# Kernel tuning notes

Hardware: AMD Instinct MI355X
Metric: run time of the kernel (lower is better)

Reference implementation:

```python
import jax, jax.numpy as jnp
import numpy as np

DECAY = 0.1
ALPHA = 0.2
EPS = 1e-8


def setup_inputs() -> dict:
    key = jax.random.key(0)
    k1, k2, k3, k4 = jax.random.split(key, 4)
    B, S, N, V = 8, 1024, 64, 32000
    input_ids = jax.random.randint(k1, (B, S), 0, V)
    emb = jax.random.normal(k2, (V, N), dtype=jnp.float32)
    W = jax.random.normal(k3, (N, N, N), dtype=jnp.float32) * 0.05
    Wd = jax.random.normal(k4, (V, N), dtype=jnp.float32) * 0.02
    bd = jnp.zeros((V,), dtype=jnp.float32)
    return {"input_ids": input_ids, "emb": emb, "W": W, "Wd": Wd, "bd": bd}


def reference(input_ids, emb, W, Wd, bd):
    B, S = input_ids.shape
    N = W.shape[0]
    # Precompute relu(embedding) for all timesteps: [B, S, N]
    word = jax.nn.relu(emb[input_ids])

    def step(hidden, w_t):
        # hidden, w_t: [B, N]
        x = (1.0 - DECAY) * hidden + w_t
        interaction = jnp.einsum('ijk,bi,bj->bk', W, x, x)
        x_act = jax.nn.relu(x + ALPHA * interaction)
        h = x_act / (jnp.sum(x_act, axis=1, keepdims=True) + EPS)
        return h, h

    h0 = jnp.zeros((B, N), dtype=emb.dtype)
    hT, hs = jax.lax.scan(step, h0, jnp.swapaxes(word, 0, 1))  # hs: [S, B, N]
    # Decode every step: Linear(N -> V): h @ Wd.T + bd -> [B, S, V]
    logits = jnp.einsum('sbn,vn->bsv', hs, Wd) + bd
    return logits, hT
```

## Files before the change

kernel.cpp:

```cpp
#include <hip/hip_runtime.h>


typedef unsigned int u32;
typedef unsigned short u16;
typedef __attribute__((ext_vector_type(8))) short short8;
typedef __attribute__((ext_vector_type(4))) float f32x4;
typedef __attribute__((ext_vector_type(4))) int i32x4;

#define DECAY_ 0.1f
#define ALPHA_ 0.2f
#define EPS_ 1e-8f
#define B_ 8
#define S_ 1024
#define N_ 64
#define V_ 32000
#define NCHUNK_ 32
#define CHUNK_ 32
#define WARM_ 24

static __device__ __forceinline__ u16 f2bf(float f) {
  u32 u = __float_as_uint(f);
  u32 r = (u + 0x7fffu + ((u >> 16) & 1u)) >> 16;
  return (u16)r;
}

#if defined(__has_builtin)
#if __has_builtin(__builtin_amdgcn_sdot4)
#define HAVE_SDOT4 1
#endif
#endif
static __device__ __forceinline__ int dot4(int a, int b, int c) {
#ifdef HAVE_SDOT4
  return __builtin_amdgcn_sdot4(a, b, c, false);
#else
  int s = c;
  s += (int)(signed char)(a) * (int)(signed char)(b);
  s += (int)(signed char)(a >> 8) * (int)(signed char)(b >> 8);
  s += (int)(signed char)(a >> 16) * (int)(signed char)(b >> 16);
  s += (int)(a >> 24) * (int)(b >> 24);
  return s;
#endif
}

static __device__ __forceinline__ float wave_max64(float v) {
#pragma unroll
  for (int m = 1; m < 64; m <<= 1) v = fmaxf(v, __shfl_xor(v, m, 64));
  return v;
}

__global__ void wmax_kernel(const float* __restrict__ W, u32* __restrict__ out) {
  int gid = blockIdx.x * blockDim.x + threadIdx.x;
  int stride = gridDim.x * blockDim.x;
  float m = 0.0f;
  for (int i = gid; i < N_ * N_ * N_; i += stride) m = fmaxf(m, fabsf(W[i]));
  m = wave_max64(m);
  if ((threadIdx.x & 63) == 0) atomicMax(out, __float_as_uint(m));
}

__global__ void quantw_kernel(const float* __restrict__ W, const u32* __restrict__ wmaxb,
                              u32* __restrict__ Wq) {
  int idx = blockIdx.x * blockDim.x + threadIdx.x;
  float s = 127.0f / fmaxf(__uint_as_float(wmaxb[0]), 1e-30f);
  int j = idx >> 10;
  int q = (idx >> 6) & 15;
  int k = idx & 63;
  u32 pk = 0;
#pragma unroll
  for (int e = 0; e < 4; ++e) {
    float v = W[(((4 * q + e) * N_) + j) * N_ + k];
    int qi = (int)rintf(v * s);
    qi = qi > 127 ? 127 : (qi < -127 ? -127 : qi);
    pk |= ((u32)qi & 0xffu) << (8 * e);
  }
  int w = j >> 3, r = j & 7;
  int jX = w * 4 + (r & 3);
  int base = (r < 4) ? 0 : 32768;
  int q4 = q >> 2, e2 = q & 3;
  Wq[base + (((jX * 4 + q4) * 64 + k) << 2) + e2] = pk;
}

__global__ void prep2_kernel(const float* __restrict__ Wd, u16* __restrict__ wdb,
                             const float* __restrict__ emb, float* __restrict__ rmax) {
  int idx = blockIdx.x * blockDim.x + threadIdx.x;
  wdb[idx] = f2bf(Wd[idx]);
  int v = blockIdx.x * 4 + (threadIdx.x >> 6);
  int lane = threadIdx.x & 63;
  float m = wave_max64(emb[(size_t)v * N_ + lane]);
  if (lane == 0) rmax[v] = fmaxf(m, 0.0f);
}

__global__ __launch_bounds__(512, 2) void recur_kernel(
    const int* __restrict__ ids, const float* __restrict__ emb,
    const u32* __restrict__ Wq, const u32* __restrict__ wmaxb,
    const float* __restrict__ rmax,
    u16* __restrict__ hs, float* __restrict__ outHT) {
  const int b = blockIdx.y;
  const int chunk = blockIdx.x;
  const int lane = threadIdx.x & 63;
  const int w = threadIdx.x >> 6;

  const int t0 = chunk * CHUNK_;
  const int ts = (chunk == 0) ? 0 : t0 - WARM_;
  const int tend = t0 + CHUNK_;

  __shared__ i32x4 lw[8192];
  __shared__ float part[8 * 64];
  __shared__ float xf_lds[N_];
  __shared__ u32 xq_lds[16];

  const float sW = __uint_as_float(wmaxb[0]) * (1.0f / 127.0f);
  const i32x4* __restrict__ WqA = (const i32x4*)Wq;

  {
    const i32x4* src = (const i32x4*)(Wq + 32768);
    for (int ii = threadIdx.x; ii < 8192; ii += 512) lw[ii] = src[ii];
  }

  float xk = 0.0f, smul = 0.0f, pend_emb = 0.0f, pend_bnd = 0.0f;
  int pend_id = 0;

  if (w == 0) {
    int id0 = ids[b * S_ + ts];
    xk = fmaxf(emb[(size_t)id0 * N_ + lane], 0.0f);
    float bnd = fmaxf(rmax[id0], 1e-20f);
    smul = bnd * (1.0f / 127.0f) * sW;
    float inv = 127.0f / bnd;
    float u = xk * inv;
    float u0 = __shfl(u, (lane & 15) * 4 + 0, 64);
    float u1 = __shfl(u, (lane & 15) * 4 + 1, 64);
    float u2 = __shfl(u, (lane & 15) * 4 + 2, 64);
    float u3 = __shfl(u, (lane & 15) * 4 + 3, 64);
    xf_lds[lane] = xk;
    if (lane < 16) {
      xq_lds[lane] = (u32)(int)rintf(u0) | ((u32)(int)rintf(u1) << 8) |
                     ((u32)(int)rintf(u2) << 16) | ((u32)(int)rintf(u3) << 24);
    }
    int i1 = ts + 1 < S_ ? ts + 1 : S_ - 1;
    int i2 = ts + 2 < S_ ? ts + 2 : S_ - 1;
    int id1 = ids[b * S_ + i1];
    pend_emb = emb[(size_t)id1 * N_ + lane];
    pend_bnd = rmax[id1];
    pend_id = ids[b * S_ + i2];
  }
  __syncthreads();

  for (int t = ts; t < tend; ++t) {
    u32 pkv = xq_lds[lane & 15];
    int xr[16];
#pragma unroll
    for (int q = 0; q < 16; ++q) xr[q] = __builtin_amdgcn_readlane((int)pkv, q);
    float pf = 0.0f;
#pragma unroll
    for (int r4 = 0; r4 < 4; ++r4) {
      int a = 0;
#pragma unroll
      for (int q4 = 0; q4 < 4; ++q4) {
        i32x4 v = lw[(((w << 2) + r4) << 2 | q4) * 64 + lane];
        a = dot4(xr[4 * q4 + 0], v[0], a);
        a = dot4(xr[4 * q4 + 1], v[1], a);
        a = dot4(xr[4 * q4 + 2], v[2], a);
        a = dot4(xr[4 * q4 + 3], v[3], a);
      }
      pf += (float)a * xf_lds[8 * w + 4 + r4];
    }
#pragma unroll
    for (int r = 0; r < 4; ++r) {
      int a = 0;
#pragma unroll
      for (int q4 = 0; q4 < 4; ++q4) {
        i32x4 v = WqA[(((w << 2) + r) << 2 | q4) * 64 + lane];
        a = dot4(xr[4 * q4 + 0], v[0], a);
        a = dot4(xr[4 * q4 + 1], v[1], a);
        a = dot4(xr[4 * q4 + 2], v[2], a);
        a = dot4(xr[4 * q4 + 3], v[3], a);
      }
      pf += (float)a * xf_lds[8 * w + r];
    }
    part[(w << 6) | lane] = pf;
    __syncthreads();

    if (w == 0) {
      float iact = 0.0f;
#pragma unroll
      for (int q = 0; q < 8; ++q) iact += part[(q << 6) | lane];
      float xact = fmaxf(fmaf(ALPHA_ * smul, iact, xk), 0.0f);
      float s = xact;
#pragma unroll
      for (int m = 1; m < 64; m <<= 1) s += __shfl_xor(s, m, 64);
      float rS = 1.0f / (s + EPS_);
      float h = xact * rS;

      if (t >= t0) {
        int mrow = b * S_ + t;
        hs[(size_t)mrow * N_ + lane] = f2bf(h);
        if (t == S_ - 1) outHT[b * N_ + lane] = h;
      }

      float wn = fmaxf(pend_emb, 0.0f);
      float xn = fmaf(1.0f - DECAY_, h, wn);
      float nbnd = (1.0f - DECAY_) + pend_bnd;
      float inv = 127.0f / nbnd;
      float u = xn * inv;
      float u0 = __shfl(u, (lane & 15) * 4 + 0, 64);
      float u1 = __shfl(u, (lane & 15) * 4 + 1, 64);
      float u2 = __shfl(u, (lane & 15) * 4 + 2, 64);
      float u3 = __shfl(u, (lane & 15) * 4 + 3, 64);
      xf_lds[lane] = xn;
      if (lane < 16) {
        xq_lds[lane] = (u32)(int)rintf(u0) | ((u32)(int)rintf(u1) << 8) |
                       ((u32)(int)rintf(u2) << 16) | ((u32)(int)rintf(u3) << 24);
      }
      smul = nbnd * (1.0f / 127.0f) * sW;
      xk = xn;

      int i2 = t + 3 < S_ ? t + 3 : S_ - 1;
      pend_emb = emb[(size_t)pend_id * N_ + lane];
      pend_bnd = rmax[pend_id];
      pend_id = ids[b * S_ + i2];
    }
    __syncthreads();
  }
}

__global__ __launch_bounds__(512, 2) void decode_kernel(
    const u16* __restrict__ hs, const u16* __restrict__ wd,
    const float* __restrict__ bd, float* __restrict__ out) {
  const int lane = threadIdx.x & 63;
  const int w = threadIdx.x >> 6;
  const int wm = w >> 2, wn = w & 3;
  const int n0 = blockIdx.x * 128 + wn * 32;
  const int m0 = blockIdx.y * 128 + wm * 64;
  const int kg = (lane >> 4) * 8;
  const int rl = lane & 15;

  short8 bfr[2][2];
#pragma unroll
  for (int nt = 0; nt < 2; ++nt) {
    int v = n0 + nt * 16 + rl;
#pragma unroll
    for (int ks = 0; ks < 2; ++ks)
      bfr[nt][ks] = *(const short8*)(wd + (size_t)v * N_ + ks * 32 + kg);
  }
  short8 a[4][2];
#pragma unroll
  for (int mt = 0; mt < 4; ++mt) {
    int row = m0 + mt * 16 + rl;
#pragma unroll
    for (int ks = 0; ks < 2; ++ks)
      a[mt][ks] = *(const short8*)(hs + (size_t)row * N_ + ks * 32 + kg);
  }
  f32x4 acc[4][2];
#pragma unroll
  for (int nt = 0; nt < 2; ++nt) {
    float bdv = bd[n0 + nt * 16 + rl];
#pragma unroll
    for (int mt = 0; mt < 4; ++mt) acc[mt][nt] = {bdv, bdv, bdv, bdv};
  }
#pragma unroll
  for (int mt = 0; mt < 4; ++mt)
#pragma unroll
    for (int nt = 0; nt < 2; ++nt) {
      acc[mt][nt] =
          __builtin_amdgcn_mfma_f32_16x16x32_bf16(a[mt][0], bfr[nt][0], acc[mt][nt], 0, 0, 0);
      acc[mt][nt] =
          __builtin_amdgcn_mfma_f32_16x16x32_bf16(a[mt][1], bfr[nt][1], acc[mt][nt], 0, 0, 0);
    }
#pragma unroll
  for (int mt = 0; mt < 4; ++mt) {
    int rbase = m0 + mt * 16 + (lane >> 4) * 4;
#pragma unroll
    for (int i = 0; i < 4; ++i) {
      float* op = out + (size_t)(rbase + i) * V_ + n0 + rl;
      __builtin_nontemporal_store(acc[mt][0][i], op);
      __builtin_nontemporal_store(acc[mt][1][i], op + 16);
    }
  }
}

extern "C" void kernel_launch(void* const* d_in, const int* in_sizes, int n_in,
                              void* d_out, int out_size, void* d_ws, size_t ws_size,
                              hipStream_t stream) {
  const int* ids = (const int*)d_in[0];
  const float* emb = (const float*)d_in[1];
  const float* W = (const float*)d_in[2];
  const float* Wd = (const float*)d_in[3];
  const float* bd = (const float*)d_in[4];
  float* out = (float*)d_out;
  char* ws = (char*)d_ws;

  u32* Wq = (u32*)(ws);
  u32* wmax = (u32*)(ws + 262144);
  float* rmax = (float*)(ws + 262208);
  u16* hs = (u16*)(ws + 390208);
  u16* wdb = (u16*)(ws + 1438784);

  hipMemsetAsync(wmax, 0, 4, stream);
  hipLaunchKernelGGL(wmax_kernel, dim3(256), dim3(256), 0, stream, W, wmax);
  hipLaunchKernelGGL(quantw_kernel, dim3(256), dim3(256), 0, stream, W, wmax, Wq);
  hipLaunchKernelGGL(prep2_kernel, dim3(8000), dim3(256), 0, stream, Wd, wdb, emb, rmax);
  hipLaunchKernelGGL(recur_kernel, dim3(NCHUNK_, B_), dim3(512), 0, stream, ids, emb,
                     Wq, wmax, rmax, hs, out + (size_t)B_ * S_ * V_);
  hipLaunchKernelGGL(decode_kernel, dim3(V_ / 128, (B_ * S_) / 128), dim3(512), 0, stream,
                     hs, wdb, bd, out);

  (void)in_sizes; (void)n_in; (void)out_size; (void)ws_size;
}
```

Baseline: 327.0 us.

## Fuse recurrence and decode into one kernel with 16-wave blocks

Merges the recurrent chunk kernel and the logits decode GEMM into one kernel. Each block keeps its 32 hidden states in LDS and decodes them against all of Wd, so the hs round trip and a launch go away. Blocks grow to 1024 threads (16 waves) to halve per-wave dot-product work per step. A dedicated wave prefetches embeddings and computes their row max, which removes the rmax precompute. Warmup shrinks from 24 to 16 steps, which cuts redundant recurrence work but may reduce the accuracy of chunk-boundary states. The decode now runs on only 256 blocks, each streaming the full Wd, which risks lower store parallelism than the separate GEMM grid.

```diff
diff --git a/kernel.cpp b/kernel.cpp
--- a/kernel.cpp
+++ b/kernel.cpp
@@ -16,7 +16,7 @@
 #define V_ 32000
 #define NCHUNK_ 32
 #define CHUNK_ 32
-#define WARM_ 24
+#define WARM_ 16
 
 static __device__ __forceinline__ u16 f2bf(float f) {
   u32 u = __float_as_uint(f);
@@ -57,43 +57,37 @@
   if ((threadIdx.x & 63) == 0) atomicMax(out, __float_as_uint(m));
 }
 
-__global__ void quantw_kernel(const float* __restrict__ W, const u32* __restrict__ wmaxb,
-                              u32* __restrict__ Wq) {
-  int idx = blockIdx.x * blockDim.x + threadIdx.x;
-  float s = 127.0f / fmaxf(__uint_as_float(wmaxb[0]), 1e-30f);
-  int j = idx >> 10;
-  int q = (idx >> 6) & 15;
-  int k = idx & 63;
-  u32 pk = 0;
-#pragma unroll
-  for (int e = 0; e < 4; ++e) {
-    float v = W[(((4 * q + e) * N_) + j) * N_ + k];
-    int qi = (int)rintf(v * s);
-    qi = qi > 127 ? 127 : (qi < -127 ? -127 : qi);
-    pk |= ((u32)qi & 0xffu) << (8 * e);
-  }
-  int w = j >> 3, r = j & 7;
-  int jX = w * 4 + (r & 3);
-  int base = (r < 4) ? 0 : 32768;
-  int q4 = q >> 2, e2 = q & 3;
-  Wq[base + (((jX * 4 + q4) * 64 + k) << 2) + e2] = pk;
-}
-
-__global__ void prep2_kernel(const float* __restrict__ Wd, u16* __restrict__ wdb,
-                             const float* __restrict__ emb, float* __restrict__ rmax) {
+__global__ void prep_kernel(const float* __restrict__ Wd, u16* __restrict__ wdb,
+                            const float* __restrict__ W, const u32* __restrict__ wmaxb,
+                            u32* __restrict__ Wq) {
   int idx = blockIdx.x * blockDim.x + threadIdx.x;
   wdb[idx] = f2bf(Wd[idx]);
-  int v = blockIdx.x * 4 + (threadIdx.x >> 6);
-  int lane = threadIdx.x & 63;
-  float m = wave_max64(emb[(size_t)v * N_ + lane]);
-  if (lane == 0) rmax[v] = fmaxf(m, 0.0f);
-}
-
-__global__ __launch_bounds__(512, 2) void recur_kernel(
+  if (blockIdx.x < 256) {
+    float s = 127.0f / fmaxf(__uint_as_float(wmaxb[0]), 1e-30f);
+    int j = idx >> 10;
+    int q = (idx >> 6) & 15;
+    int k = idx & 63;
+    u32 pk = 0;
+#pragma unroll
+    for (int e = 0; e < 4; ++e) {
+      float v = W[(((4 * q + e) * N_) + j) * N_ + k];
+      int qi = (int)rintf(v * s);
+      qi = qi > 127 ? 127 : (qi < -127 ? -127 : qi);
+      pk |= ((u32)qi & 0xffu) << (8 * e);
+    }
+    int g = j >> 2, r = j & 3;
+    int jX = g * 2 + (r & 1);
+    int base = (r < 2) ? 0 : 32768;
+    int q4 = q >> 2, e2 = q & 3;
+    Wq[base + (((jX * 4 + q4) * 64 + k) << 2) + e2] = pk;
+  }
+}
+
+__global__ __launch_bounds__(1024, 4) void fused_kernel(
     const int* __restrict__ ids, const float* __restrict__ emb,
     const u32* __restrict__ Wq, const u32* __restrict__ wmaxb,
-    const float* __restrict__ rmax,
-    u16* __restrict__ hs, float* __restrict__ outHT) {
+    const u16* __restrict__ wdb, const float* __restrict__ bd,
+    float* __restrict__ out, float* __restrict__ outHT) {
   const int b = blockIdx.y;
   const int chunk = blockIdx.x;
   const int lane = threadIdx.x & 63;
@@ -104,25 +98,27 @@
   const int tend = t0 + CHUNK_;
 
   __shared__ i32x4 lw[8192];
-  __shared__ float part[8 * 64];
+  __shared__ float part[16 * 64];
   __shared__ float xf_lds[N_];
   __shared__ u32 xq_lds[16];
+  __shared__ float pend_w[2][N_];
+  __shared__ float pend_b[2];
+  __shared__ u16 hsl[CHUNK_][68];
 
   const float sW = __uint_as_float(wmaxb[0]) * (1.0f / 127.0f);
   const i32x4* __restrict__ WqA = (const i32x4*)Wq;
 
   {
     const i32x4* src = (const i32x4*)(Wq + 32768);
-    for (int ii = threadIdx.x; ii < 8192; ii += 512) lw[ii] = src[ii];
-  }
-
-  float xk = 0.0f, smul = 0.0f, pend_emb = 0.0f, pend_bnd = 0.0f;
-  int pend_id = 0;
+    for (int ii = threadIdx.x; ii < 8192; ii += 1024) lw[ii] = src[ii];
+  }
+
+  float xk = 0.0f, smul = 0.0f;
 
   if (w == 0) {
     int id0 = ids[b * S_ + ts];
     xk = fmaxf(emb[(size_t)id0 * N_ + lane], 0.0f);
-    float bnd = fmaxf(rmax[id0], 1e-20f);
+    float bnd = fmaxf(wave_max64(xk), 1e-20f);
     smul = bnd * (1.0f / 127.0f) * sW;
     float inv = 127.0f / bnd;
     float u = xk * inv;
@@ -135,46 +131,53 @@
       xq_lds[lane] = (u32)(int)rintf(u0) | ((u32)(int)rintf(u1) << 8) |
                      ((u32)(int)rintf(u2) << 16) | ((u32)(int)rintf(u3) << 24);
     }
+  }
+  if (w == 1) {
     int i1 = ts + 1 < S_ ? ts + 1 : S_ - 1;
-    int i2 = ts + 2 < S_ ? ts + 2 : S_ - 1;
     int id1 = ids[b * S_ + i1];
-    pend_emb = emb[(size_t)id1 * N_ + lane];
-    pend_bnd = rmax[id1];
-    pend_id = ids[b * S_ + i2];
+    float pv = fmaxf(emb[(size_t)id1 * N_ + lane], 0.0f);
+    float pm = wave_max64(pv);
+    pend_w[(ts + 1) & 1][lane] = pv;
+    if (lane == 0) pend_b[(ts + 1) & 1] = pm;
   }
   __syncthreads();
 
   for (int t = ts; t < tend; ++t) {
+    float pv = 0.0f;
+    if (w == 1) {
+      int i2 = t + 2 < S_ ? t + 2 : S_ - 1;
+      pv = emb[(size_t)ids[b * S_ + i2] * N_ + lane];
+    }
     u32 pkv = xq_lds[lane & 15];
     int xr[16];
 #pragma unroll
     for (int q = 0; q < 16; ++q) xr[q] = __builtin_amdgcn_readlane((int)pkv, q);
     float pf = 0.0f;
 #pragma unroll
-    for (int r4 = 0; r4 < 4; ++r4) {
+    for (int rr = 0; rr < 2; ++rr) {
       int a = 0;
 #pragma unroll
       for (int q4 = 0; q4 < 4; ++q4) {
-        i32x4 v = lw[(((w << 2) + r4) << 2 | q4) * 64 + lane];
+        i32x4 v = lw[((2 * w + rr) * 4 + q4) * 64 + lane];
         a = dot4(xr[4 * q4 + 0], v[0], a);
         a = dot4(xr[4 * q4 + 1], v[1], a);
         a = dot4(xr[4 * q4 + 2], v[2], a);
         a = dot4(xr[4 * q4 + 3], v[3], a);
       }
-      pf += (float)a * xf_lds[8 * w + 4 + r4];
-    }
-#pragma unroll
-    for (int r = 0; r < 4; ++r) {
+      pf += (float)a * xf_lds[4 * w + 2 + rr];
+    }
+#pragma unroll
+    for (int rr = 0; rr < 2; ++rr) {
       int a = 0;
 #pragma unroll
       for (int q4 = 0; q4 < 4; ++q4) {
-        i32x4 v = WqA[(((w << 2) + r) << 2 | q4) * 64 + lane];
+        i32x4 v = WqA[((2 * w + rr) * 4 + q4) * 64 + lane];
         a = dot4(xr[4 * q4 + 0], v[0], a);
         a = dot4(xr[4 * q4 + 1], v[1], a);
         a = dot4(xr[4 * q4 + 2], v[2], a);
         a = dot4(xr[4 * q4 + 3], v[3], a);
       }
-      pf += (float)a * xf_lds[8 * w + r];
+      pf += (float)a * xf_lds[4 * w + rr];
     }
     part[(w << 6) | lane] = pf;
     __syncthreads();
@@ -182,7 +185,7 @@
     if (w == 0) {
       float iact = 0.0f;
 #pragma unroll
-      for (int q = 0; q < 8; ++q) iact += part[(q << 6) | lane];
+      for (int q = 0; q < 16; ++q) iact += part[(q << 6) | lane];
       float xact = fmaxf(fmaf(ALPHA_ * smul, iact, xk), 0.0f);
       float s = xact;
 #pragma unroll
@@ -191,14 +194,14 @@
       float h = xact * rS;
 
       if (t >= t0) {
-        int mrow = b * S_ + t;
-        hs[(size_t)mrow * N_ + lane] = f2bf(h);
+        hsl[t - t0][lane] = f2bf(h);
         if (t == S_ - 1) outHT[b * N_ + lane] = h;
       }
 
-      float wn = fmaxf(pend_emb, 0.0f);
+      int rs = (t + 1) & 1;
+      float wn = pend_w[rs][lane];
       float xn = fmaf(1.0f - DECAY_, h, wn);
-      float nbnd = (1.0f - DECAY_) + pend_bnd;
+      float nbnd = (1.0f - DECAY_) + pend_b[rs];
       float inv = 127.0f / nbnd;
       float u = xn * inv;
       float u0 = __shfl(u, (lane & 15) * 4 + 0, 64);
@@ -212,67 +215,41 @@
       }
       smul = nbnd * (1.0f / 127.0f) * sW;
       xk = xn;
-
-      int i2 = t + 3 < S_ ? t + 3 : S_ - 1;
-      pend_emb = emb[(size_t)pend_id * N_ + lane];
-      pend_bnd = rmax[pend_id];
-      pend_id = ids[b * S_ + i2];
+    } else if (w == 1) {
+      float pr = fmaxf(pv, 0.0f);
+      float pm = wave_max64(pr);
+      pend_w[t & 1][lane] = pr;
+      if (lane == 0) pend_b[t & 1] = pm;
     }
     __syncthreads();
   }
-}
-
-__global__ __launch_bounds__(512, 2) void decode_kernel(
-    const u16* __restrict__ hs, const u16* __restrict__ wd,
-    const float* __restrict__ bd, float* __restrict__ out) {
-  const int lane = threadIdx.x & 63;
-  const int w = threadIdx.x >> 6;
-  const int wm = w >> 2, wn = w & 3;
-  const int n0 = blockIdx.x * 128 + wn * 32;
-  const int m0 = blockIdx.y * 128 + wm * 64;
-  const int kg = (lane >> 4) * 8;
-  const int rl = lane & 15;
-
-  short8 bfr[2][2];
-#pragma unroll
-  for (int nt = 0; nt < 2; ++nt) {
-    int v = n0 + nt * 16 + rl;
+
+  const int rl = lane & 15, g = lane >> 4, kg = g * 8;
+  short8 afr[2][2];
+#pragma unroll
+  for (int mt = 0; mt < 2; ++mt)
 #pragma unroll
     for (int ks = 0; ks < 2; ++ks)
-      bfr[nt][ks] = *(const short8*)(wd + (size_t)v * N_ + ks * 32 + kg);
-  }
-  short8 a[4][2];
-#pragma unroll
-  for (int mt = 0; mt < 4; ++mt) {
-    int row = m0 + mt * 16 + rl;
-#pragma unroll
-    for (int ks = 0; ks < 2; ++ks)
-      a[mt][ks] = *(const short8*)(hs + (size_t)row * N_ + ks * 32 + kg);
-  }
-  f32x4 acc[4][2];
-#pragma unroll
-  for (int nt = 0; nt < 2; ++nt) {
-    float bdv = bd[n0 + nt * 16 + rl];
-#pragma unroll
-    for (int mt = 0; mt < 4; ++mt) acc[mt][nt] = {bdv, bdv, bdv, bdv};
-  }
-#pragma unroll
-  for (int mt = 0; mt < 4; ++mt)
-#pragma unroll
-    for (int nt = 0; nt < 2; ++nt) {
-      acc[mt][nt] =
-          __builtin_amdgcn_mfma_f32_16x16x32_bf16(a[mt][0], bfr[nt][0], acc[mt][nt], 0, 0, 0);
-      acc[mt][nt] =
-          __builtin_amdgcn_mfma_f32_16x16x32_bf16(a[mt][1], bfr[nt][1], acc[mt][nt], 0, 0, 0);
-    }
-#pragma unroll
-  for (int mt = 0; mt < 4; ++mt) {
-    int rbase = m0 + mt * 16 + (lane >> 4) * 4;
+      afr[mt][ks] = *(const short8*)&hsl[mt * 16 + rl][ks * 32 + kg];
+
+  const size_t mbase = (size_t)b * S_ + t0;
+  const int colbase = w * (V_ / 16);
+#pragma unroll 1
+  for (int tile = 0; tile < V_ / 16 / 16; ++tile) {
+    int col = colbase + tile * 16 + rl;
+    short8 b0 = *(const short8*)(wdb + (size_t)col * N_ + kg);
+    short8 b1 = *(const short8*)(wdb + (size_t)col * N_ + 32 + kg);
+    float bdv = bd[col];
+    f32x4 acc0 = {bdv, bdv, bdv, bdv};
+    f32x4 acc1 = acc0;
+    acc0 = __builtin_amdgcn_mfma_f32_16x16x32_bf16(afr[0][0], b0, acc0, 0, 0, 0);
+    acc0 = __builtin_amdgcn_mfma_f32_16x16x32_bf16(afr[0][1], b1, acc0, 0, 0, 0);
+    acc1 = __builtin_amdgcn_mfma_f32_16x16x32_bf16(afr[1][0], b0, acc1, 0, 0, 0);
+    acc1 = __builtin_amdgcn_mfma_f32_16x16x32_bf16(afr[1][1], b1, acc1, 0, 0, 0);
 #pragma unroll
     for (int i = 0; i < 4; ++i) {
-      float* op = out + (size_t)(rbase + i) * V_ + n0 + rl;
-      __builtin_nontemporal_store(acc[mt][0][i], op);
-      __builtin_nontemporal_store(acc[mt][1][i], op + 16);
+      __builtin_nontemporal_store(acc0[i], out + (mbase + g * 4 + i) * V_ + col);
+      __builtin_nontemporal_store(acc1[i], out + (mbase + 16 + g * 4 + i) * V_ + col);
     }
   }
 }
@@ -290,18 +267,13 @@
 
   u32* Wq = (u32*)(ws);
   u32* wmax = (u32*)(ws + 262144);
-  float* rmax = (float*)(ws + 262208);
-  u16* hs = (u16*)(ws + 390208);
-  u16* wdb = (u16*)(ws + 1438784);
+  u16* wdb = (u16*)(ws + 262208);
 
   hipMemsetAsync(wmax, 0, 4, stream);
   hipLaunchKernelGGL(wmax_kernel, dim3(256), dim3(256), 0, stream, W, wmax);
-  hipLaunchKernelGGL(quantw_kernel, dim3(256), dim3(256), 0, stream, W, wmax, Wq);
-  hipLaunchKernelGGL(prep2_kernel, dim3(8000), dim3(256), 0, stream, Wd, wdb, emb, rmax);
-  hipLaunchKernelGGL(recur_kernel, dim3(NCHUNK_, B_), dim3(512), 0, stream, ids, emb,
-                     Wq, wmax, rmax, hs, out + (size_t)B_ * S_ * V_);
-  hipLaunchKernelGGL(decode_kernel, dim3(V_ / 128, (B_ * S_) / 128), dim3(512), 0, stream,
-                     hs, wdb, bd, out);
+  hipLaunchKernelGGL(prep_kernel, dim3(8000), dim3(256), 0, stream, Wd, wdb, W, wmax, Wq);
+  hipLaunchKernelGGL(fused_kernel, dim3(NCHUNK_, B_), dim3(1024), 0, stream, ids, emb,
+                     Wq, wmax, wdb, bd, out, out + (size_t)B_ * S_ * V_);
 
   (void)in_sizes; (void)n_in; (void)out_size; (void)ws_size;
 }
```

Measured after the change: 437.1 us. 1.34x slower.
